# Optimization experiments

Hardware: AMD Instinct MI355X
Metric: run time of the kernel (lower is better)

The kernel has to match this reference:

```python
import jax, jax.numpy as jnp
import numpy as np

EMBED = 768
HIDDEN = 768
HEADS = 12
HEAD_DIM = HIDDEN // HEADS
B, S = 4, 2048


def setup_inputs() -> dict:
    key = jax.random.key(0)
    ks = jax.random.split(key, 12)
    sd = 1.0 / np.sqrt(EMBED)
    return {
        "vector1": jax.random.normal(ks[0], (B, S, EMBED), jnp.float32),
        "vector2": jax.random.normal(ks[1], (B, S, EMBED), jnp.float32),
        "Wq": jax.random.normal(ks[2], (HIDDEN, EMBED), jnp.float32) * sd,
        "bq": jnp.zeros((HIDDEN,), jnp.float32),
        "Wk": jax.random.normal(ks[3], (HIDDEN, EMBED), jnp.float32) * sd,
        "bk": jnp.zeros((HIDDEN,), jnp.float32),
        "Wv": jax.random.normal(ks[4], (HIDDEN, EMBED), jnp.float32) * sd,
        "bv": jnp.zeros((HIDDEN,), jnp.float32),
        "Wo": jax.random.normal(ks[5], (EMBED, HIDDEN), jnp.float32) * sd,
        "bo": jnp.zeros((EMBED,), jnp.float32),
        "alpha": jnp.float32(0.5),
        "beta": jnp.float32(0.5),
    }


def reference(vector1, vector2, Wq, bq, Wk, bk, Wv, bv, Wo, bo, alpha, beta):
    b, s, _ = vector1.shape
    # Linear projections (torch Linear: x @ W.T + b)
    Q = (vector1 @ Wq.T + bq).reshape(b, s, HEADS, HEAD_DIM)  # [B,S,H,D]
    K = (vector2 @ Wk.T + bk).reshape(b, s, HEADS, HEAD_DIM)
    V = (vector2 @ Wv.T + bv).reshape(b, s, HEADS, HEAD_DIM)
    # NOTE: module scales by sqrt(hidden_dim), NOT sqrt(head_dim)
    scale = jnp.float32(np.sqrt(HIDDEN))
    scores = jnp.einsum("bqhd,bkhd->bhqk", Q / scale, K)  # [B,H,S,S]
    # max-subtract + softmax == numerically stable softmax
    attn = jax.nn.softmax(scores, axis=-1)
    out = jnp.einsum("bhqk,bkhd->bqhd", attn, V).reshape(b, s, HIDDEN)
    adjusted = vector1 @ Wo.T + bo
    return alpha * out + beta * adjusted
```

## Files before the change

### kernel.cpp

```cpp
#include <hip/hip_runtime.h>
#include <hip/hip_bf16.h>

#define LOG2E 1.4426950408889634f

typedef __attribute__((ext_vector_type(4)))  float f32x4;
typedef __attribute__((ext_vector_type(16))) float f32x16;
typedef __attribute__((ext_vector_type(8)))  short s16x8;
typedef __attribute__((ext_vector_type(8)))  unsigned short u16x8_t;
typedef __attribute__((ext_vector_type(4)))  int i32x4;

static __device__ __forceinline__ unsigned short f2b(float f) {
    __hip_bfloat16 h = __float2bfloat16(f);
    return __builtin_bit_cast(unsigned short, h);
}

static __device__ __forceinline__ void gload_lds16(const unsigned short* g, unsigned short* l) {
    __builtin_amdgcn_global_load_lds(
        (const __attribute__((address_space(1))) void*)g,
        (__attribute__((address_space(3))) void*)l, 16, 0, 0);
}

__global__ void cvt_f32_to_bf16(const float* __restrict__ src,
                                unsigned short* __restrict__ dst, int n4) {
    int i = blockIdx.x * blockDim.x + threadIdx.x;
    int stride = gridDim.x * blockDim.x;
    for (; i < n4; i += stride) {
        f32x4 v = reinterpret_cast<const f32x4*>(src)[i];
        ushort4 o;
        o.x = f2b(v.x); o.y = f2b(v.y); o.z = f2b(v.z); o.w = f2b(v.w);
        reinterpret_cast<ushort4*>(dst)[i] = o;
    }
}

__global__ void cvt_weights(const float* __restrict__ wq, const float* __restrict__ wk,
                            const float* __restrict__ wv, const float* __restrict__ wo,
                            unsigned short* __restrict__ dst, int quarter4) {
    int i = blockIdx.x * blockDim.x + threadIdx.x;
    int seg = i / quarter4;
    int j = i - seg * quarter4;
    const float* src = (seg == 0) ? wq : (seg == 1) ? wk : (seg == 2) ? wv : wo;
    f32x4 v = reinterpret_cast<const f32x4*>(src)[j];
    ushort4 o;
    o.x = f2b(v.x); o.y = f2b(v.y); o.z = f2b(v.z); o.w = f2b(v.w);
    reinterpret_cast<ushort4*>(dst)[i] = o;
}

__global__ __launch_bounds__(256) void gemm_qkvo(
    const unsigned short* __restrict__ A1,
    const unsigned short* __restrict__ A2,
    const unsigned short* __restrict__ Wcat,
    const float* __restrict__ bq, const float* __restrict__ bk,
    const float* __restrict__ bv, const float* __restrict__ bo,
    unsigned short* __restrict__ Qb,
    unsigned short* __restrict__ Kb,
    unsigned short* __restrict__ Vtb,
    float* __restrict__ adj,
    float qscale)
{
    __shared__ unsigned short As[128 * 64];
    __shared__ unsigned short Bs[128 * 64];

    const int n0g = blockIdx.x * 128;
    const int seg = blockIdx.x / 6;
    const int n0 = n0g - seg * 768;
    const int m0 = blockIdx.y * 128;
    const unsigned short* A = (seg == 1 || seg == 2) ? A2 : A1;
    const float* bias = (seg == 0) ? bq : (seg == 1) ? bk : (seg == 2) ? bv : bo;

    const int tid = threadIdx.x;
    const int w = tid >> 6, lane = tid & 63;
    const int lg = lane >> 4, lr = lane & 15;
    const int wm = w >> 1, wn = w & 1;
    const int srow = tid >> 3;
    const int scol = (tid & 7) * 8;

    const unsigned short* Ag = A    + (size_t)(m0  + srow) * 768 + scol;
    const unsigned short* Bg = Wcat + (size_t)(n0g + srow) * 768 + scol;
    unsigned short* Al = &As[tid * 8];
    unsigned short* Bl = &Bs[tid * 8];

    f32x4 acc[4][4];
#pragma unroll
    for (int i = 0; i < 4; i++)
#pragma unroll
        for (int j = 0; j < 4; j++) acc[i][j] = f32x4{0.f, 0.f, 0.f, 0.f};

    for (int k0 = 0; k0 < 768; k0 += 64) {
#pragma unroll
        for (int c = 0; c < 4; c++) {
            gload_lds16(Ag + c * 32 * 768 + k0, Al + c * 2048);
            gload_lds16(Bg + c * 32 * 768 + k0, Bl + c * 2048);
        }
        __syncthreads();
#pragma unroll
        for (int kk = 0; kk < 2; ++kk) {
            s16x8 af[4], bf[4];
#pragma unroll
            for (int mi = 0; mi < 4; mi++)
                af[mi] = *reinterpret_cast<const s16x8*>(&As[(wm * 64 + mi * 16 + lr) * 64 + kk * 32 + lg * 8]);
#pragma unroll
            for (int ni = 0; ni < 4; ni++)
                bf[ni] = *reinterpret_cast<const s16x8*>(&Bs[(wn * 64 + ni * 16 + lr) * 64 + kk * 32 + lg * 8]);
#pragma unroll
            for (int mi = 0; mi < 4; mi++)
#pragma unroll
                for (int ni = 0; ni < 4; ni++)
                    acc[mi][ni] = __builtin_amdgcn_mfma_f32_16x16x32_bf16(af[mi], bf[ni], acc[mi][ni], 0, 0, 0);
        }
        __syncthreads();
    }

#pragma unroll
    for (int ni = 0; ni < 4; ni++) {
        int n = n0 + wn * 64 + ni * 16 + lr;
        float bn = bias[n];
#pragma unroll
        for (int mi = 0; mi < 4; mi++) {
#pragma unroll
            for (int i = 0; i < 4; i++) {
                int m = m0 + wm * 64 + mi * 16 + 4 * lg + i;
                float v = acc[mi][ni][i] + bn;
                if (seg == 0) {
                    Qb[(size_t)m * 768 + n] = f2b(v * qscale);
                } else if (seg == 1) {
                    Kb[(size_t)m * 768 + n] = f2b(v);
                } else if (seg == 2) {
                    int bb = m >> 11, ss = m & 2047;
                    Vtb[((size_t)(bb * 768 + n) << 11) + ss] = f2b(v);
                } else {
                    adj[(size_t)m * 768 + n] = v;
                }
            }
        }
    }
}

__global__ __launch_bounds__(256, 3) void attn_fused(
    const unsigned short* __restrict__ Qb,
    const unsigned short* __restrict__ Kb,
    const unsigned short* __restrict__ Vt,
    const float* __restrict__ adj,
    const float* __restrict__ alpha_p,
    const float* __restrict__ beta_p,
    float* __restrict__ out)
{
    __shared__ unsigned short Ksm[2][64][72];
    __shared__ unsigned short Vsm[2][64][72];

    const int bh = blockIdx.x;
    const int b = bh / 12, h = bh - 12 * (bh / 12);
    const int tid = threadIdx.x, w = tid >> 6, lane = tid & 63;
    const int ql = lane & 31, hi = lane >> 5;
    const int q0 = blockIdx.y * 128 + w * 32;

    const size_t qbase = ((size_t)(b * 2048 + q0 + ql)) * 768 + h * 64;
    s16x8 qreg[4];
#pragma unroll
    for (int ds = 0; ds < 4; ds++)
        qreg[ds] = *reinterpret_cast<const s16x8*>(Qb + qbase + ds * 16 + hi * 8);

    f32x16 z16;
#pragma unroll
    for (int r = 0; r < 16; r++) z16[r] = 0.f;
    f32x16 acc[2];
#pragma unroll
    for (int dd = 0; dd < 2; dd++) acc[dd] = z16;
    float l = 0.f;

    const size_t kbase = (size_t)b * 2048 * 768 + (size_t)h * 64;
    const size_t vbase = (size_t)(b * 768 + h * 64) * 2048;

    const int krow = tid >> 3, kc8 = (tid & 7) * 8;
    const int vrow = tid >> 3, vc8 = (tid & 7) * 8;

    u16x8_t kst[2], vst[2];
    auto load_tile = [&](int t0) {
#pragma unroll
        for (int i = 0; i < 2; i++)
            kst[i] = *reinterpret_cast<const u16x8_t*>(Kb + kbase + (size_t)(t0 + i * 32 + krow) * 768 + kc8);
#pragma unroll
        for (int i = 0; i < 2; i++)
            vst[i] = *reinterpret_cast<const u16x8_t*>(Vt + vbase + (size_t)(i * 32 + vrow) * 2048 + t0 + vc8);
    };
    auto write_tile = [&](int buf) {
#pragma unroll
        for (int i = 0; i < 2; i++)
            *reinterpret_cast<u16x8_t*>(&Ksm[buf][i * 32 + krow][kc8]) = kst[i];
#pragma unroll
        for (int i = 0; i < 2; i++)
            *reinterpret_cast<u16x8_t*>(&Vsm[buf][i * 32 + vrow][vc8]) = vst[i];
    };

    load_tile(0);
    write_tile(0);
    load_tile(64);
    __syncthreads();

#pragma unroll 1
    for (int t = 0; t < 32; t++) {
        const int cur = t & 1;
        if (t + 1 < 32) write_tile(cur ^ 1);
        if (t + 2 < 32) load_tile((t + 2) * 64);

#pragma unroll
        for (int kb2 = 0; kb2 < 2; kb2++) {
            s16x8 ka0 = *reinterpret_cast<const s16x8*>(&Ksm[cur][kb2 * 32 + ql][0 * 16 + hi * 8]);
            s16x8 ka1 = *reinterpret_cast<const s16x8*>(&Ksm[cur][kb2 * 32 + ql][1 * 16 + hi * 8]);
            s16x8 ka2 = *reinterpret_cast<const s16x8*>(&Ksm[cur][kb2 * 32 + ql][2 * 16 + hi * 8]);
            s16x8 ka3 = *reinterpret_cast<const s16x8*>(&Ksm[cur][kb2 * 32 + ql][3 * 16 + hi * 8]);
            __builtin_amdgcn_s_setprio(1);
            f32x16 sc = __builtin_amdgcn_mfma_f32_32x32x16_bf16(ka0, qreg[0], z16, 0, 0, 0);
            sc = __builtin_amdgcn_mfma_f32_32x32x16_bf16(ka1, qreg[1], sc, 0, 0, 0);
            sc = __builtin_amdgcn_mfma_f32_32x32x16_bf16(ka2, qreg[2], sc, 0, 0, 0);
            sc = __builtin_amdgcn_mfma_f32_32x32x16_bf16(ka3, qreg[3], sc, 0, 0, 0);
            __builtin_amdgcn_s_setprio(0);

            float p[16];
#pragma unroll
            for (int r = 0; r < 16; r++) p[r] = __builtin_exp2f(sc[r]);
            {
                float s0 = p[0] + p[1],  s1 = p[2] + p[3],  s2 = p[4] + p[5],  s3 = p[6] + p[7];
                float s4 = p[8] + p[9],  s5 = p[10] + p[11], s6 = p[12] + p[13], s7 = p[14] + p[15];
                float t0a = s0 + s1, t1a = s2 + s3, t2a = s4 + s5, t3a = s6 + s7;
                l += (t0a + t1a) + (t2a + t3a);
            }

            s16x8 pf[2];
            {
                unsigned int a0, b0, a1, b1, a2, b2, a3, b3;
                asm("v_cvt_pk_bf16_f32 %0, %1, %2" : "=v"(a0) : "v"(p[0]),  "v"(p[1]));
                asm("v_cvt_pk_bf16_f32 %0, %1, %2" : "=v"(b0) : "v"(p[4]),  "v"(p[5]));
                asm("v_cvt_pk_bf16_f32 %0, %1, %2" : "=v"(a1) : "v"(p[2]),  "v"(p[3]));
                asm("v_cvt_pk_bf16_f32 %0, %1, %2" : "=v"(b1) : "v"(p[6]),  "v"(p[7]));
                asm("v_cvt_pk_bf16_f32 %0, %1, %2" : "=v"(a2) : "v"(p[8]),  "v"(p[9]));
                asm("v_cvt_pk_bf16_f32 %0, %1, %2" : "=v"(b2) : "v"(p[12]), "v"(p[13]));
                asm("v_cvt_pk_bf16_f32 %0, %1, %2" : "=v"(a3) : "v"(p[10]), "v"(p[11]));
                asm("v_cvt_pk_bf16_f32 %0, %1, %2" : "=v"(b3) : "v"(p[14]), "v"(p[15]));
                asm volatile("v_permlane32_swap_b32 %0, %1" : "+v"(a0), "+v"(b0));
                asm volatile("v_permlane32_swap_b32 %0, %1" : "+v"(a1), "+v"(b1));
                asm volatile("v_permlane32_swap_b32 %0, %1" : "+v"(a2), "+v"(b2));
                asm volatile("v_permlane32_swap_b32 %0, %1" : "+v"(a3), "+v"(b3));
                i32x4 w0; w0[0] = (int)a0; w0[1] = (int)a1; w0[2] = (int)b0; w0[3] = (int)b1;
                i32x4 w1; w1[0] = (int)a2; w1[1] = (int)a3; w1[2] = (int)b2; w1[3] = (int)b3;
                pf[0] = __builtin_bit_cast(s16x8, w0);
                pf[1] = __builtin_bit_cast(s16x8, w1);
            }

            s16x8 va00 = *reinterpret_cast<const s16x8*>(&Vsm[cur][0 * 32 + ql][kb2 * 32 + 0 * 16 + hi * 8]);
            s16x8 va01 = *reinterpret_cast<const s16x8*>(&Vsm[cur][1 * 32 + ql][kb2 * 32 + 0 * 16 + hi * 8]);
            s16x8 va10 = *reinterpret_cast<const s16x8*>(&Vsm[cur][0 * 32 + ql][kb2 * 32 + 1 * 16 + hi * 8]);
            s16x8 va11 = *reinterpret_cast<const s16x8*>(&Vsm[cur][1 * 32 + ql][kb2 * 32 + 1 * 16 + hi * 8]);
            __builtin_amdgcn_s_setprio(1);
            acc[0] = __builtin_amdgcn_mfma_f32_32x32x16_bf16(va00, pf[0], acc[0], 0, 0, 0);
            acc[1] = __builtin_amdgcn_mfma_f32_32x32x16_bf16(va01, pf[0], acc[1], 0, 0, 0);
            acc[0] = __builtin_amdgcn_mfma_f32_32x32x16_bf16(va10, pf[1], acc[0], 0, 0, 0);
            acc[1] = __builtin_amdgcn_mfma_f32_32x32x16_bf16(va11, pf[1], acc[1], 0, 0, 0);
            __builtin_amdgcn_s_setprio(0);
        }
        __syncthreads();
    }

    l += __shfl_xor(l, 32, 64);

    const float alpha = *alpha_p, beta = *beta_p;
    const float s = alpha / l;
#pragma unroll
    for (int dd = 0; dd < 2; dd++) {
#pragma unroll
        for (int rg = 0; rg < 4; rg++) {
            int d0 = dd * 32 + rg * 8 + hi * 4;
            size_t idx = qbase + d0;
            f32x4 av = *reinterpret_cast<const f32x4*>(adj + idx);
            f32x4 o;
#pragma unroll
            for (int i = 0; i < 4; i++)
                o[i] = acc[dd][rg * 4 + i] * s + beta * av[i];
            *reinterpret_cast<f32x4*>(out + idx) = o;
        }
    }
}

extern "C" void kernel_launch(void* const* d_in, const int* in_sizes, int n_in,
                              void* d_out, int out_size, void* d_ws, size_t ws_size,
                              hipStream_t stream) {
    const float* v1 = (const float*)d_in[0];
    const float* v2 = (const float*)d_in[1];
    const float* Wq = (const float*)d_in[2];
    const float* bq = (const float*)d_in[3];
    const float* Wk = (const float*)d_in[4];
    const float* bk = (const float*)d_in[5];
    const float* Wv = (const float*)d_in[6];
    const float* bv = (const float*)d_in[7];
    const float* Wo = (const float*)d_in[8];
    const float* bo = (const float*)d_in[9];
    const float* alpha = (const float*)d_in[10];
    const float* beta = (const float*)d_in[11];
    float* out = (float*)d_out;

    const size_t ACT = (size_t)8192 * 768;
    const size_t WSZ = (size_t)768 * 768;
    char* ws = (char*)d_ws;
    size_t off = 0;
    auto alloc = [&](size_t bytes) {
        char* p = ws + off;
        off += (bytes + 255) & ~(size_t)255;
        return p;
    };
    unsigned short* v1b  = (unsigned short*)alloc(ACT * 2);
    unsigned short* v2b  = (unsigned short*)alloc(ACT * 2);
    unsigned short* wcat = (unsigned short*)alloc(4 * WSZ * 2);
    unsigned short* Qb   = (unsigned short*)alloc(ACT * 2);
    unsigned short* Kb   = (unsigned short*)alloc(ACT * 2);
    unsigned short* Vtb  = (unsigned short*)alloc(ACT * 2);
    float* adj = (float*)alloc(ACT * 4);

    cvt_f32_to_bf16<<<dim3(1024), dim3(256), 0, stream>>>(v1, v1b, (int)(ACT / 4));
    cvt_f32_to_bf16<<<dim3(1024), dim3(256), 0, stream>>>(v2, v2b, (int)(ACT / 4));
    cvt_weights<<<dim3((int)(4 * WSZ / 4 / 256)), dim3(256), 0, stream>>>(
        Wq, Wk, Wv, Wo, wcat, (int)(WSZ / 4));

    const float qscale = 0.03608439182435161f * 1.4426950408889634f;
    gemm_qkvo<<<dim3(24, 64), dim3(256), 0, stream>>>(
        v1b, v2b, wcat, bq, bk, bv, bo, Qb, Kb, Vtb, adj, qscale);

    attn_fused<<<dim3(48, 16), dim3(256), 0, stream>>>(Qb, Kb, Vtb, adj, alpha, beta, out);
}
```

Baseline: 289.6 us.

## Double-buffer GEMM LDS, remap GEMM blocks across XCDs, give attention waves two query tiles

The QKVO GEMM now uses two LDS buffers, so the next K-slice is staged while the current one is multiplied. It also launches as a 1D grid whose block IDs are remapped so consecutive blocks land on the same XCD. The attention kernel drops to 128 threads, and each wave handles two 32-query fragments. This lets each K/V fragment read from LDS feed twice as many MFMAs, cutting LDS traffic per unit of work. In exchange, register pressure rises and there are fewer waves per CU to hide latency.

```diff
diff --git a/kernel.cpp b/kernel.cpp
--- a/kernel.cpp
+++ b/kernel.cpp
@@ -57,13 +57,17 @@
     float* __restrict__ adj,
     float qscale)
 {
-    __shared__ unsigned short As[128 * 64];
-    __shared__ unsigned short Bs[128 * 64];
-
-    const int n0g = blockIdx.x * 128;
-    const int seg = blockIdx.x / 6;
+    __shared__ unsigned short As[2][128 * 64];
+    __shared__ unsigned short Bs[2][128 * 64];
+
+    const int bid = blockIdx.x;
+    const int wg = (bid & 7) * 192 + (bid >> 3);
+    const int mblk = wg / 24;
+    const int nblk = wg - mblk * 24;
+    const int n0g = nblk * 128;
+    const int seg = nblk / 6;
     const int n0 = n0g - seg * 768;
-    const int m0 = blockIdx.y * 128;
+    const int m0 = mblk * 128;
     const unsigned short* A = (seg == 1 || seg == 2) ? A2 : A1;
     const float* bias = (seg == 0) ? bq : (seg == 1) ? bk : (seg == 2) ? bv : bo;
 
@@ -76,8 +80,14 @@
 
     const unsigned short* Ag = A    + (size_t)(m0  + srow) * 768 + scol;
     const unsigned short* Bg = Wcat + (size_t)(n0g + srow) * 768 + scol;
-    unsigned short* Al = &As[tid * 8];
-    unsigned short* Bl = &Bs[tid * 8];
+
+    auto STAGE = [&](int buf, int k0) {
+#pragma unroll
+        for (int c = 0; c < 4; c++) {
+            gload_lds16(Ag + c * 32 * 768 + k0, &As[buf][tid * 8 + c * 2048]);
+            gload_lds16(Bg + c * 32 * 768 + k0, &Bs[buf][tid * 8 + c * 2048]);
+        }
+    };
 
     f32x4 acc[4][4];
 #pragma unroll
@@ -85,22 +95,22 @@
 #pragma unroll
         for (int j = 0; j < 4; j++) acc[i][j] = f32x4{0.f, 0.f, 0.f, 0.f};
 
-    for (int k0 = 0; k0 < 768; k0 += 64) {
-#pragma unroll
-        for (int c = 0; c < 4; c++) {
-            gload_lds16(Ag + c * 32 * 768 + k0, Al + c * 2048);
-            gload_lds16(Bg + c * 32 * 768 + k0, Bl + c * 2048);
-        }
-        __syncthreads();
+    STAGE(0, 0);
+    __syncthreads();
+
+#pragma unroll 1
+    for (int t = 0; t < 12; t++) {
+        const int curb = t & 1;
+        if (t + 1 < 12) STAGE(curb ^ 1, (t + 1) * 64);
 #pragma unroll
         for (int kk = 0; kk < 2; ++kk) {
             s16x8 af[4], bf[4];
 #pragma unroll
             for (int mi = 0; mi < 4; mi++)
-                af[mi] = *reinterpret_cast<const s16x8*>(&As[(wm * 64 + mi * 16 + lr) * 64 + kk * 32 + lg * 8]);
+                af[mi] = *reinterpret_cast<const s16x8*>(&As[curb][(wm * 64 + mi * 16 + lr) * 64 + kk * 32 + lg * 8]);
 #pragma unroll
             for (int ni = 0; ni < 4; ni++)
-                bf[ni] = *reinterpret_cast<const s16x8*>(&Bs[(wn * 64 + ni * 16 + lr) * 64 + kk * 32 + lg * 8]);
+                bf[ni] = *reinterpret_cast<const s16x8*>(&Bs[curb][(wn * 64 + ni * 16 + lr) * 64 + kk * 32 + lg * 8]);
 #pragma unroll
             for (int mi = 0; mi < 4; mi++)
 #pragma unroll
@@ -135,7 +145,7 @@
     }
 }
 
-__global__ __launch_bounds__(256, 3) void attn_fused(
+__global__ __launch_bounds__(128, 2) void attn_fused(
     const unsigned short* __restrict__ Qb,
     const unsigned short* __restrict__ Kb,
     const unsigned short* __restrict__ Vt,
@@ -151,44 +161,47 @@
     const int b = bh / 12, h = bh - 12 * (bh / 12);
     const int tid = threadIdx.x, w = tid >> 6, lane = tid & 63;
     const int ql = lane & 31, hi = lane >> 5;
-    const int q0 = blockIdx.y * 128 + w * 32;
+    const int q0 = blockIdx.y * 128 + w * 64;
 
     const size_t qbase = ((size_t)(b * 2048 + q0 + ql)) * 768 + h * 64;
-    s16x8 qreg[4];
-#pragma unroll
-    for (int ds = 0; ds < 4; ds++)
-        qreg[ds] = *reinterpret_cast<const s16x8*>(Qb + qbase + ds * 16 + hi * 8);
+    s16x8 qreg[2][4];
+#pragma unroll
+    for (int qf = 0; qf < 2; qf++)
+#pragma unroll
+        for (int ds = 0; ds < 4; ds++)
+            qreg[qf][ds] = *reinterpret_cast<const s16x8*>(Qb + qbase + (size_t)qf * 32 * 768 + ds * 16 + hi * 8);
 
     f32x16 z16;
 #pragma unroll
     for (int r = 0; r < 16; r++) z16[r] = 0.f;
-    f32x16 acc[2];
-#pragma unroll
-    for (int dd = 0; dd < 2; dd++) acc[dd] = z16;
-    float l = 0.f;
+    f32x16 acc[2][2];
+#pragma unroll
+    for (int qf = 0; qf < 2; qf++)
+#pragma unroll
+        for (int dd = 0; dd < 2; dd++) acc[qf][dd] = z16;
+    float l0 = 0.f, l1 = 0.f;
 
     const size_t kbase = (size_t)b * 2048 * 768 + (size_t)h * 64;
     const size_t vbase = (size_t)(b * 768 + h * 64) * 2048;
 
     const int krow = tid >> 3, kc8 = (tid & 7) * 8;
-    const int vrow = tid >> 3, vc8 = (tid & 7) * 8;
-
-    u16x8_t kst[2], vst[2];
+
+    u16x8_t kst[4], vst[4];
     auto load_tile = [&](int t0) {
 #pragma unroll
-        for (int i = 0; i < 2; i++)
-            kst[i] = *reinterpret_cast<const u16x8_t*>(Kb + kbase + (size_t)(t0 + i * 32 + krow) * 768 + kc8);
-#pragma unroll
-        for (int i = 0; i < 2; i++)
-            vst[i] = *reinterpret_cast<const u16x8_t*>(Vt + vbase + (size_t)(i * 32 + vrow) * 2048 + t0 + vc8);
+        for (int i = 0; i < 4; i++)
+            kst[i] = *reinterpret_cast<const u16x8_t*>(Kb + kbase + (size_t)(t0 + i * 16 + krow) * 768 + kc8);
+#pragma unroll
+        for (int i = 0; i < 4; i++)
+            vst[i] = *reinterpret_cast<const u16x8_t*>(Vt + vbase + (size_t)(i * 16 + krow) * 2048 + t0 + kc8);
     };
     auto write_tile = [&](int buf) {
 #pragma unroll
-        for (int i = 0; i < 2; i++)
-            *reinterpret_cast<u16x8_t*>(&Ksm[buf][i * 32 + krow][kc8]) = kst[i];
-#pragma unroll
-        for (int i = 0; i < 2; i++)
-            *reinterpret_cast<u16x8_t*>(&Vsm[buf][i * 32 + vrow][vc8]) = vst[i];
+        for (int i = 0; i < 4; i++)
+            *reinterpret_cast<u16x8_t*>(&Ksm[buf][i * 16 + krow][kc8]) = kst[i];
+#pragma unroll
+        for (int i = 0; i < 4; i++)
+            *reinterpret_cast<u16x8_t*>(&Vsm[buf][i * 16 + krow][kc8]) = vst[i];
     };
 
     load_tile(0);
@@ -208,74 +221,84 @@
             s16x8 ka1 = *reinterpret_cast<const s16x8*>(&Ksm[cur][kb2 * 32 + ql][1 * 16 + hi * 8]);
             s16x8 ka2 = *reinterpret_cast<const s16x8*>(&Ksm[cur][kb2 * 32 + ql][2 * 16 + hi * 8]);
             s16x8 ka3 = *reinterpret_cast<const s16x8*>(&Ksm[cur][kb2 * 32 + ql][3 * 16 + hi * 8]);
-            __builtin_amdgcn_s_setprio(1);
-            f32x16 sc = __builtin_amdgcn_mfma_f32_32x32x16_bf16(ka0, qreg[0], z16, 0, 0, 0);
-            sc = __builtin_amdgcn_mfma_f32_32x32x16_bf16(ka1, qreg[1], sc, 0, 0, 0);
-            sc = __builtin_amdgcn_mfma_f32_32x32x16_bf16(ka2, qreg[2], sc, 0, 0, 0);
-            sc = __builtin_amdgcn_mfma_f32_32x32x16_bf16(ka3, qreg[3], sc, 0, 0, 0);
-            __builtin_amdgcn_s_setprio(0);
-
-            float p[16];
-#pragma unroll
-            for (int r = 0; r < 16; r++) p[r] = __builtin_exp2f(sc[r]);
-            {
-                float s0 = p[0] + p[1],  s1 = p[2] + p[3],  s2 = p[4] + p[5],  s3 = p[6] + p[7];
-                float s4 = p[8] + p[9],  s5 = p[10] + p[11], s6 = p[12] + p[13], s7 = p[14] + p[15];
-                float t0a = s0 + s1, t1a = s2 + s3, t2a = s4 + s5, t3a = s6 + s7;
-                l += (t0a + t1a) + (t2a + t3a);
-            }
-
-            s16x8 pf[2];
-            {
-                unsigned int a0, b0, a1, b1, a2, b2, a3, b3;
-                asm("v_cvt_pk_bf16_f32 %0, %1, %2" : "=v"(a0) : "v"(p[0]),  "v"(p[1]));
-                asm("v_cvt_pk_bf16_f32 %0, %1, %2" : "=v"(b0) : "v"(p[4]),  "v"(p[5]));
-                asm("v_cvt_pk_bf16_f32 %0, %1, %2" : "=v"(a1) : "v"(p[2]),  "v"(p[3]));
-                asm("v_cvt_pk_bf16_f32 %0, %1, %2" : "=v"(b1) : "v"(p[6]),  "v"(p[7]));
-                asm("v_cvt_pk_bf16_f32 %0, %1, %2" : "=v"(a2) : "v"(p[8]),  "v"(p[9]));
-                asm("v_cvt_pk_bf16_f32 %0, %1, %2" : "=v"(b2) : "v"(p[12]), "v"(p[13]));
-                asm("v_cvt_pk_bf16_f32 %0, %1, %2" : "=v"(a3) : "v"(p[10]), "v"(p[11]));
-                asm("v_cvt_pk_bf16_f32 %0, %1, %2" : "=v"(b3) : "v"(p[14]), "v"(p[15]));
-                asm volatile("v_permlane32_swap_b32 %0, %1" : "+v"(a0), "+v"(b0));
-                asm volatile("v_permlane32_swap_b32 %0, %1" : "+v"(a1), "+v"(b1));
-                asm volatile("v_permlane32_swap_b32 %0, %1" : "+v"(a2), "+v"(b2));
-                asm volatile("v_permlane32_swap_b32 %0, %1" : "+v"(a3), "+v"(b3));
-                i32x4 w0; w0[0] = (int)a0; w0[1] = (int)a1; w0[2] = (int)b0; w0[3] = (int)b1;
-                i32x4 w1; w1[0] = (int)a2; w1[1] = (int)a3; w1[2] = (int)b2; w1[3] = (int)b3;
-                pf[0] = __builtin_bit_cast(s16x8, w0);
-                pf[1] = __builtin_bit_cast(s16x8, w1);
-            }
-
             s16x8 va00 = *reinterpret_cast<const s16x8*>(&Vsm[cur][0 * 32 + ql][kb2 * 32 + 0 * 16 + hi * 8]);
             s16x8 va01 = *reinterpret_cast<const s16x8*>(&Vsm[cur][1 * 32 + ql][kb2 * 32 + 0 * 16 + hi * 8]);
             s16x8 va10 = *reinterpret_cast<const s16x8*>(&Vsm[cur][0 * 32 + ql][kb2 * 32 + 1 * 16 + hi * 8]);
             s16x8 va11 = *reinterpret_cast<const s16x8*>(&Vsm[cur][1 * 32 + ql][kb2 * 32 + 1 * 16 + hi * 8]);
-            __builtin_amdgcn_s_setprio(1);
-            acc[0] = __builtin_amdgcn_mfma_f32_32x32x16_bf16(va00, pf[0], acc[0], 0, 0, 0);
-            acc[1] = __builtin_amdgcn_mfma_f32_32x32x16_bf16(va01, pf[0], acc[1], 0, 0, 0);
-            acc[0] = __builtin_amdgcn_mfma_f32_32x32x16_bf16(va10, pf[1], acc[0], 0, 0, 0);
-            acc[1] = __builtin_amdgcn_mfma_f32_32x32x16_bf16(va11, pf[1], acc[1], 0, 0, 0);
-            __builtin_amdgcn_s_setprio(0);
+
+#pragma unroll
+            for (int qf = 0; qf < 2; qf++) {
+                __builtin_amdgcn_s_setprio(1);
+                f32x16 sc = __builtin_amdgcn_mfma_f32_32x32x16_bf16(ka0, qreg[qf][0], z16, 0, 0, 0);
+                sc = __builtin_amdgcn_mfma_f32_32x32x16_bf16(ka1, qreg[qf][1], sc, 0, 0, 0);
+                sc = __builtin_amdgcn_mfma_f32_32x32x16_bf16(ka2, qreg[qf][2], sc, 0, 0, 0);
+                sc = __builtin_amdgcn_mfma_f32_32x32x16_bf16(ka3, qreg[qf][3], sc, 0, 0, 0);
+                __builtin_amdgcn_s_setprio(0);
+
+                float p[16];
+#pragma unroll
+                for (int r = 0; r < 16; r++) p[r] = __builtin_exp2f(sc[r]);
+                {
+                    float s0 = p[0] + p[1],  s1 = p[2] + p[3],  s2 = p[4] + p[5],  s3 = p[6] + p[7];
+                    float s4 = p[8] + p[9],  s5 = p[10] + p[11], s6 = p[12] + p[13], s7 = p[14] + p[15];
+                    float t0a = s0 + s1, t1a = s2 + s3, t2a = s4 + s5, t3a = s6 + s7;
+                    float ls = (t0a + t1a) + (t2a + t3a);
+                    if (qf) l1 += ls; else l0 += ls;
+                }
+
+                s16x8 pf0, pf1;
+                {
+                    unsigned int a0, b0, a1, b1, a2, b2, a3, b3;
+                    asm("v_cvt_pk_bf16_f32 %0, %1, %2" : "=v"(a0) : "v"(p[0]),  "v"(p[1]));
+                    asm("v_cvt_pk_bf16_f32 %0, %1, %2" : "=v"(b0) : "v"(p[4]),  "v"(p[5]));
+                    asm("v_cvt_pk_bf16_f32 %0, %1, %2" : "=v"(a1) : "v"(p[2]),  "v"(p[3]));
+                    asm("v_cvt_pk_bf16_f32 %0, %1, %2" : "=v"(b1) : "v"(p[6]),  "v"(p[7]));
+                    asm("v_cvt_pk_bf16_f32 %0, %1, %2" : "=v"(a2) : "v"(p[8]),  "v"(p[9]));
+                    asm("v_cvt_pk_bf16_f32 %0, %1, %2" : "=v"(b2) : "v"(p[12]), "v"(p[13]));
+                    asm("v_cvt_pk_bf16_f32 %0, %1, %2" : "=v"(a3) : "v"(p[10]), "v"(p[11]));
+                    asm("v_cvt_pk_bf16_f32 %0, %1, %2" : "=v"(b3) : "v"(p[14]), "v"(p[15]));
+                    asm volatile("v_permlane32_swap_b32 %0, %1" : "+v"(a0), "+v"(b0));
+                    asm volatile("v_permlane32_swap_b32 %0, %1" : "+v"(a1), "+v"(b1));
+                    asm volatile("v_permlane32_swap_b32 %0, %1" : "+v"(a2), "+v"(b2));
+                    asm volatile("v_permlane32_swap_b32 %0, %1" : "+v"(a3), "+v"(b3));
+                    i32x4 w0; w0[0] = (int)a0; w0[1] = (int)a1; w0[2] = (int)b0; w0[3] = (int)b1;
+                    i32x4 w1; w1[0] = (int)a2; w1[1] = (int)a3; w1[2] = (int)b2; w1[3] = (int)b3;
+                    pf0 = __builtin_bit_cast(s16x8, w0);
+                    pf1 = __builtin_bit_cast(s16x8, w1);
+                }
+
+                __builtin_amdgcn_s_setprio(1);
+                acc[qf][0] = __builtin_amdgcn_mfma_f32_32x32x16_bf16(va00, pf0, acc[qf][0], 0, 0, 0);
+                acc[qf][1] = __builtin_amdgcn_mfma_f32_32x32x16_bf16(va01, pf0, acc[qf][1], 0, 0, 0);
+                acc[qf][0] = __builtin_amdgcn_mfma_f32_32x32x16_bf16(va10, pf1, acc[qf][0], 0, 0, 0);
+                acc[qf][1] = __builtin_amdgcn_mfma_f32_32x32x16_bf16(va11, pf1, acc[qf][1], 0, 0, 0);
+                __builtin_amdgcn_s_setprio(0);
+            }
         }
         __syncthreads();
     }
 
-    l += __shfl_xor(l, 32, 64);
+    l0 += __shfl_xor(l0, 32, 64);
+    l1 += __shfl_xor(l1, 32, 64);
 
     const float alpha = *alpha_p, beta = *beta_p;
-    const float s = alpha / l;
-#pragma unroll
-    for (int dd = 0; dd < 2; dd++) {
-#pragma unroll
-        for (int rg = 0; rg < 4; rg++) {
-            int d0 = dd * 32 + rg * 8 + hi * 4;
-            size_t idx = qbase + d0;
-            f32x4 av = *reinterpret_cast<const f32x4*>(adj + idx);
-            f32x4 o;
-#pragma unroll
-            for (int i = 0; i < 4; i++)
-                o[i] = acc[dd][rg * 4 + i] * s + beta * av[i];
-            *reinterpret_cast<f32x4*>(out + idx) = o;
+    const float s0v = alpha / l0, s1v = alpha / l1;
+#pragma unroll
+    for (int qf = 0; qf < 2; qf++) {
+        const float sv = qf ? s1v : s0v;
+#pragma unroll
+        for (int dd = 0; dd < 2; dd++) {
+#pragma unroll
+            for (int rg = 0; rg < 4; rg++) {
+                int d0 = dd * 32 + rg * 8 + hi * 4;
+                size_t idx = qbase + (size_t)qf * 32 * 768 + d0;
+                f32x4 av = *reinterpret_cast<const f32x4*>(adj + idx);
+                f32x4 o;
+#pragma unroll
+                for (int i = 0; i < 4; i++)
+                    o[i] = acc[qf][dd][rg * 4 + i] * sv + beta * av[i];
+                *reinterpret_cast<f32x4*>(out + idx) = o;
+            }
         }
     }
 }
@@ -320,8 +343,8 @@
         Wq, Wk, Wv, Wo, wcat, (int)(WSZ / 4));
 
     const float qscale = 0.03608439182435161f * 1.4426950408889634f;
-    gemm_qkvo<<<dim3(24, 64), dim3(256), 0, stream>>>(
+    gemm_qkvo<<<dim3(1536), dim3(256), 0, stream>>>(
         v1b, v2b, wcat, bq, bk, bv, bo, Qb, Kb, Vtb, adj, qscale);
 
-    attn_fused<<<dim3(48, 16), dim3(256), 0, stream>>>(Qb, Kb, Vtb, adj, alpha, beta, out);
-}
+    attn_fused<<<dim3(48, 16), dim3(128), 0, stream>>>(Qb, Kb, Vtb, adj, alpha, beta, out);
+}
```

Result: slower. 309.9 us (+7.0%).

## Split attention over KV halves, double-buffer GEMM LDS, remap GEMM block order

Applied to the files above, without the earlier changes.

Attention is split along the key dimension into two halves (grid z=2), each writing unnormalized partial outputs and row sums. A new combine kernel adds them, normalizes, and applies the alpha/beta blend with the adjusted projection. This doubles the number of attention blocks for better CU occupancy, at the cost of an extra pass over fp32 partials. The projection GEMM now double-buffers its LDS tiles so the next k-slice loads while the current one computes. It also remaps block ids so neighbouring blocks share L2 data, and reuses dead workspace buffers for the partials.

```diff
diff --git a/kernel.cpp b/kernel.cpp
--- a/kernel.cpp
+++ b/kernel.cpp
@@ -1,7 +1,5 @@
 #include <hip/hip_runtime.h>
 #include <hip/hip_bf16.h>
-
-#define LOG2E 1.4426950408889634f
 
 typedef __attribute__((ext_vector_type(4)))  float f32x4;
 typedef __attribute__((ext_vector_type(16))) float f32x16;
@@ -57,13 +55,17 @@
     float* __restrict__ adj,
     float qscale)
 {
-    __shared__ unsigned short As[128 * 64];
-    __shared__ unsigned short Bs[128 * 64];
-
-    const int n0g = blockIdx.x * 128;
-    const int seg = blockIdx.x / 6;
+    __shared__ unsigned short As[2][128 * 64];
+    __shared__ unsigned short Bs[2][128 * 64];
+
+    const int bid = blockIdx.x;
+    const int wg = (bid & 7) * 192 + (bid >> 3);
+    const int mblk = wg / 24;
+    const int nblk = wg - mblk * 24;
+    const int n0g = nblk * 128;
+    const int seg = nblk / 6;
     const int n0 = n0g - seg * 768;
-    const int m0 = blockIdx.y * 128;
+    const int m0 = mblk * 128;
     const unsigned short* A = (seg == 1 || seg == 2) ? A2 : A1;
     const float* bias = (seg == 0) ? bq : (seg == 1) ? bk : (seg == 2) ? bv : bo;
 
@@ -76,8 +78,14 @@
 
     const unsigned short* Ag = A    + (size_t)(m0  + srow) * 768 + scol;
     const unsigned short* Bg = Wcat + (size_t)(n0g + srow) * 768 + scol;
-    unsigned short* Al = &As[tid * 8];
-    unsigned short* Bl = &Bs[tid * 8];
+
+    auto STAGE = [&](int buf, int k0) {
+#pragma unroll
+        for (int c = 0; c < 4; c++) {
+            gload_lds16(Ag + c * 32 * 768 + k0, &As[buf][tid * 8 + c * 2048]);
+            gload_lds16(Bg + c * 32 * 768 + k0, &Bs[buf][tid * 8 + c * 2048]);
+        }
+    };
 
     f32x4 acc[4][4];
 #pragma unroll
@@ -85,22 +93,22 @@
 #pragma unroll
         for (int j = 0; j < 4; j++) acc[i][j] = f32x4{0.f, 0.f, 0.f, 0.f};
 
-    for (int k0 = 0; k0 < 768; k0 += 64) {
-#pragma unroll
-        for (int c = 0; c < 4; c++) {
-            gload_lds16(Ag + c * 32 * 768 + k0, Al + c * 2048);
-            gload_lds16(Bg + c * 32 * 768 + k0, Bl + c * 2048);
-        }
-        __syncthreads();
+    STAGE(0, 0);
+    __syncthreads();
+
+#pragma unroll 1
+    for (int t = 0; t < 12; t++) {
+        const int curb = t & 1;
+        if (t + 1 < 12) STAGE(curb ^ 1, (t + 1) * 64);
 #pragma unroll
         for (int kk = 0; kk < 2; ++kk) {
             s16x8 af[4], bf[4];
 #pragma unroll
             for (int mi = 0; mi < 4; mi++)
-                af[mi] = *reinterpret_cast<const s16x8*>(&As[(wm * 64 + mi * 16 + lr) * 64 + kk * 32 + lg * 8]);
+                af[mi] = *reinterpret_cast<const s16x8*>(&As[curb][(wm * 64 + mi * 16 + lr) * 64 + kk * 32 + lg * 8]);
 #pragma unroll
             for (int ni = 0; ni < 4; ni++)
-                bf[ni] = *reinterpret_cast<const s16x8*>(&Bs[(wn * 64 + ni * 16 + lr) * 64 + kk * 32 + lg * 8]);
+                bf[ni] = *reinterpret_cast<const s16x8*>(&Bs[curb][(wn * 64 + ni * 16 + lr) * 64 + kk * 32 + lg * 8]);
 #pragma unroll
             for (int mi = 0; mi < 4; mi++)
 #pragma unroll
@@ -135,20 +143,25 @@
     }
 }
 
-__global__ __launch_bounds__(256, 3) void attn_fused(
+__global__ __launch_bounds__(256, 4) void attn_partial(
     const unsigned short* __restrict__ Qb,
     const unsigned short* __restrict__ Kb,
     const unsigned short* __restrict__ Vt,
-    const float* __restrict__ adj,
-    const float* __restrict__ alpha_p,
-    const float* __restrict__ beta_p,
-    float* __restrict__ out)
+    float* __restrict__ po0,
+    float* __restrict__ po1,
+    float* __restrict__ lp0,
+    float* __restrict__ lp1)
 {
     __shared__ unsigned short Ksm[2][64][72];
     __shared__ unsigned short Vsm[2][64][72];
 
     const int bh = blockIdx.x;
     const int b = bh / 12, h = bh - 12 * (bh / 12);
+    const int z = blockIdx.z;
+    const int tb = z << 10;
+    float* __restrict__ po = z ? po1 : po0;
+    float* __restrict__ lp = z ? lp1 : lp0;
+
     const int tid = threadIdx.x, w = tid >> 6, lane = tid & 63;
     const int ql = lane & 31, hi = lane >> 5;
     const int q0 = blockIdx.y * 128 + w * 32;
@@ -171,7 +184,6 @@
     const size_t vbase = (size_t)(b * 768 + h * 64) * 2048;
 
     const int krow = tid >> 3, kc8 = (tid & 7) * 8;
-    const int vrow = tid >> 3, vc8 = (tid & 7) * 8;
 
     u16x8_t kst[2], vst[2];
     auto load_tile = [&](int t0) {
@@ -180,7 +192,7 @@
             kst[i] = *reinterpret_cast<const u16x8_t*>(Kb + kbase + (size_t)(t0 + i * 32 + krow) * 768 + kc8);
 #pragma unroll
         for (int i = 0; i < 2; i++)
-            vst[i] = *reinterpret_cast<const u16x8_t*>(Vt + vbase + (size_t)(i * 32 + vrow) * 2048 + t0 + vc8);
+            vst[i] = *reinterpret_cast<const u16x8_t*>(Vt + vbase + (size_t)(i * 32 + krow) * 2048 + t0 + kc8);
     };
     auto write_tile = [&](int buf) {
 #pragma unroll
@@ -188,19 +200,19 @@
             *reinterpret_cast<u16x8_t*>(&Ksm[buf][i * 32 + krow][kc8]) = kst[i];
 #pragma unroll
         for (int i = 0; i < 2; i++)
-            *reinterpret_cast<u16x8_t*>(&Vsm[buf][i * 32 + vrow][vc8]) = vst[i];
+            *reinterpret_cast<u16x8_t*>(&Vsm[buf][i * 32 + krow][kc8]) = vst[i];
     };
 
-    load_tile(0);
+    load_tile(tb);
     write_tile(0);
-    load_tile(64);
+    load_tile(tb + 64);
     __syncthreads();
 
 #pragma unroll 1
-    for (int t = 0; t < 32; t++) {
+    for (int t = 0; t < 16; t++) {
         const int cur = t & 1;
-        if (t + 1 < 32) write_tile(cur ^ 1);
-        if (t + 2 < 32) load_tile((t + 2) * 64);
+        if (t + 1 < 16) write_tile(cur ^ 1);
+        if (t + 2 < 16) load_tile(tb + (t + 2) * 64);
 
 #pragma unroll
         for (int kb2 = 0; kb2 < 2; kb2++) {
@@ -262,22 +274,41 @@
 
     l += __shfl_xor(l, 32, 64);
 
-    const float alpha = *alpha_p, beta = *beta_p;
-    const float s = alpha / l;
 #pragma unroll
     for (int dd = 0; dd < 2; dd++) {
 #pragma unroll
         for (int rg = 0; rg < 4; rg++) {
             int d0 = dd * 32 + rg * 8 + hi * 4;
-            size_t idx = qbase + d0;
-            f32x4 av = *reinterpret_cast<const f32x4*>(adj + idx);
             f32x4 o;
 #pragma unroll
-            for (int i = 0; i < 4; i++)
-                o[i] = acc[dd][rg * 4 + i] * s + beta * av[i];
-            *reinterpret_cast<f32x4*>(out + idx) = o;
-        }
-    }
+            for (int i = 0; i < 4; i++) o[i] = acc[dd][rg * 4 + i];
+            *reinterpret_cast<f32x4*>(po + qbase + d0) = o;
+        }
+    }
+    if (lane < 32) lp[(b * 2048 + q0 + ql) * 12 + h] = l;
+}
+
+__global__ __launch_bounds__(256) void combine_out(
+    const float* __restrict__ po1,
+    const float* __restrict__ lp0, const float* __restrict__ lp1,
+    const float* __restrict__ adj,
+    const float* __restrict__ alpha_p, const float* __restrict__ beta_p,
+    float* __restrict__ out)
+{
+    int i = blockIdx.x * 256 + threadIdx.x;
+    int q = i / 192;
+    int c = i - q * 192;
+    int h = c >> 4;
+    float l = lp0[q * 12 + h] + lp1[q * 12 + h];
+    const float s = (*alpha_p) / l;
+    const float beta = *beta_p;
+    f32x4 a = reinterpret_cast<const f32x4*>(out)[i];
+    f32x4 bq = reinterpret_cast<const f32x4*>(po1)[i];
+    f32x4 ad = reinterpret_cast<const f32x4*>(adj)[i];
+    f32x4 o;
+#pragma unroll
+    for (int j = 0; j < 4; j++) o[j] = (a[j] + bq[j]) * s + beta * ad[j];
+    reinterpret_cast<f32x4*>(out)[i] = o;
 }
 
 extern "C" void kernel_launch(void* const* d_in, const int* in_sizes, int n_in,
@@ -314,14 +345,23 @@
     unsigned short* Vtb  = (unsigned short*)alloc(ACT * 2);
     float* adj = (float*)alloc(ACT * 4);
 
+    float* po1 = (float*)v1b;
+    float* lp0 = (float*)wcat;
+    float* lp1 = lp0 + 8192 * 12;
+    float* po0 = out;
+
     cvt_f32_to_bf16<<<dim3(1024), dim3(256), 0, stream>>>(v1, v1b, (int)(ACT / 4));
     cvt_f32_to_bf16<<<dim3(1024), dim3(256), 0, stream>>>(v2, v2b, (int)(ACT / 4));
     cvt_weights<<<dim3((int)(4 * WSZ / 4 / 256)), dim3(256), 0, stream>>>(
         Wq, Wk, Wv, Wo, wcat, (int)(WSZ / 4));
 
     const float qscale = 0.03608439182435161f * 1.4426950408889634f;
-    gemm_qkvo<<<dim3(24, 64), dim3(256), 0, stream>>>(
+    gemm_qkvo<<<dim3(1536), dim3(256), 0, stream>>>(
         v1b, v2b, wcat, bq, bk, bv, bo, Qb, Kb, Vtb, adj, qscale);
 
-    attn_fused<<<dim3(48, 16), dim3(256), 0, stream>>>(Qb, Kb, Vtb, adj, alpha, beta, out);
-}
+    attn_partial<<<dim3(48, 16, 2), dim3(256), 0, stream>>>(
+        Qb, Kb, Vtb, po0, po1, lp0, lp1);
+
+    combine_out<<<dim3(6144), dim3(256), 0, stream>>>(
+        po1, lp0, lp1, adj, alpha, beta, out);
+}
```

New measurement: 322.4 us. +11.3%, slower.

## Pipeline QKVO GEMM loads in a 4-stage ring, swizzle blocks, compute softmax sum via MFMA

Applied to the files above, without the earlier changes.

The projection GEMM now stages K-slices of 32 through a four-buffer LDS ring using async global-to-LDS loads. It waits on vmcnt counters so loads overlap with MFMA work, instead of syncing twice per 64-wide step. Block IDs are remapped across XCDs so neighbouring tiles share L2. In attention, the softmax row sum moves from VALU adds to an extra MFMA against a ones vector. This trades more matrix-core work for fewer vector instructions and drops the cross-lane shuffle, but the row sum is now accumulated from bf16-rounded probabilities.

```diff
diff --git a/kernel.cpp b/kernel.cpp
--- a/kernel.cpp
+++ b/kernel.cpp
@@ -1,7 +1,5 @@
 #include <hip/hip_runtime.h>
 #include <hip/hip_bf16.h>
-
-#define LOG2E 1.4426950408889634f
 
 typedef __attribute__((ext_vector_type(4)))  float f32x4;
 typedef __attribute__((ext_vector_type(16))) float f32x16;
@@ -57,13 +55,17 @@
     float* __restrict__ adj,
     float qscale)
 {
-    __shared__ unsigned short As[128 * 64];
-    __shared__ unsigned short Bs[128 * 64];
-
-    const int n0g = blockIdx.x * 128;
-    const int seg = blockIdx.x / 6;
+    __shared__ unsigned short As[4 * 128 * 32];
+    __shared__ unsigned short Bs[4 * 128 * 32];
+
+    const int bid = blockIdx.x;
+    const int wg = (bid & 7) * 192 + (bid >> 3);
+    const int mblk = wg / 24;
+    const int nblk = wg - mblk * 24;
+    const int n0g = nblk * 128;
+    const int seg = nblk / 6;
     const int n0 = n0g - seg * 768;
-    const int m0 = blockIdx.y * 128;
+    const int m0 = mblk * 128;
     const unsigned short* A = (seg == 1 || seg == 2) ? A2 : A1;
     const float* bias = (seg == 0) ? bq : (seg == 1) ? bk : (seg == 2) ? bv : bo;
 
@@ -71,13 +73,19 @@
     const int w = tid >> 6, lane = tid & 63;
     const int lg = lane >> 4, lr = lane & 15;
     const int wm = w >> 1, wn = w & 1;
-    const int srow = tid >> 3;
-    const int scol = (tid & 7) * 8;
+    const int srow = tid >> 2;
+    const int scol = (tid & 3) * 8;
 
     const unsigned short* Ag = A    + (size_t)(m0  + srow) * 768 + scol;
     const unsigned short* Bg = Wcat + (size_t)(n0g + srow) * 768 + scol;
-    unsigned short* Al = &As[tid * 8];
-    unsigned short* Bl = &Bs[tid * 8];
+
+    auto STAGE = [&](int buf, int k0) {
+#pragma unroll
+        for (int c = 0; c < 2; c++) {
+            gload_lds16(Ag + (size_t)c * 64 * 768 + k0, &As[buf * 4096 + tid * 8 + c * 2048]);
+            gload_lds16(Bg + (size_t)c * 64 * 768 + k0, &Bs[buf * 4096 + tid * 8 + c * 2048]);
+        }
+    };
 
     f32x4 acc[4][4];
 #pragma unroll
@@ -85,30 +93,41 @@
 #pragma unroll
         for (int j = 0; j < 4; j++) acc[i][j] = f32x4{0.f, 0.f, 0.f, 0.f};
 
-    for (int k0 = 0; k0 < 768; k0 += 64) {
-#pragma unroll
-        for (int c = 0; c < 4; c++) {
-            gload_lds16(Ag + c * 32 * 768 + k0, Al + c * 2048);
-            gload_lds16(Bg + c * 32 * 768 + k0, Bl + c * 2048);
-        }
-        __syncthreads();
-#pragma unroll
-        for (int kk = 0; kk < 2; ++kk) {
-            s16x8 af[4], bf[4];
-#pragma unroll
-            for (int mi = 0; mi < 4; mi++)
-                af[mi] = *reinterpret_cast<const s16x8*>(&As[(wm * 64 + mi * 16 + lr) * 64 + kk * 32 + lg * 8]);
+    auto COMPUTE = [&](int buf) {
+        s16x8 af[4], bf[4];
+#pragma unroll
+        for (int mi = 0; mi < 4; mi++)
+            af[mi] = *reinterpret_cast<const s16x8*>(&As[buf * 4096 + (wm * 64 + mi * 16 + lr) * 32 + lg * 8]);
+#pragma unroll
+        for (int ni = 0; ni < 4; ni++)
+            bf[ni] = *reinterpret_cast<const s16x8*>(&Bs[buf * 4096 + (wn * 64 + ni * 16 + lr) * 32 + lg * 8]);
+#pragma unroll
+        for (int mi = 0; mi < 4; mi++)
 #pragma unroll
             for (int ni = 0; ni < 4; ni++)
-                bf[ni] = *reinterpret_cast<const s16x8*>(&Bs[(wn * 64 + ni * 16 + lr) * 64 + kk * 32 + lg * 8]);
-#pragma unroll
-            for (int mi = 0; mi < 4; mi++)
-#pragma unroll
-                for (int ni = 0; ni < 4; ni++)
-                    acc[mi][ni] = __builtin_amdgcn_mfma_f32_16x16x32_bf16(af[mi], bf[ni], acc[mi][ni], 0, 0, 0);
-        }
-        __syncthreads();
-    }
+                acc[mi][ni] = __builtin_amdgcn_mfma_f32_16x16x32_bf16(af[mi], bf[ni], acc[mi][ni], 0, 0, 0);
+    };
+
+    STAGE(0, 0);
+    STAGE(1, 32);
+    STAGE(2, 64);
+
+#pragma unroll 1
+    for (int t = 0; t < 22; t++) {
+        asm volatile("s_waitcnt vmcnt(8)" ::: "memory");
+        __builtin_amdgcn_sched_barrier(0);
+        __builtin_amdgcn_s_barrier();
+        if (t + 3 < 24) STAGE((t + 3) & 3, (t + 3) * 32);
+        COMPUTE(t & 3);
+    }
+    asm volatile("s_waitcnt vmcnt(4)" ::: "memory");
+    __builtin_amdgcn_sched_barrier(0);
+    __builtin_amdgcn_s_barrier();
+    COMPUTE(22 & 3);
+    asm volatile("s_waitcnt vmcnt(0)" ::: "memory");
+    __builtin_amdgcn_sched_barrier(0);
+    __builtin_amdgcn_s_barrier();
+    COMPUTE(23 & 3);
 
 #pragma unroll
     for (int ni = 0; ni < 4; ni++) {
@@ -159,19 +178,22 @@
     for (int ds = 0; ds < 4; ds++)
         qreg[ds] = *reinterpret_cast<const s16x8*>(Qb + qbase + ds * 16 + hi * 8);
 
+    s16x8 ones;
+#pragma unroll
+    for (int j = 0; j < 8; j++) ones[j] = (short)0x3F80;
+
     f32x16 z16;
 #pragma unroll
     for (int r = 0; r < 16; r++) z16[r] = 0.f;
     f32x16 acc[2];
 #pragma unroll
     for (int dd = 0; dd < 2; dd++) acc[dd] = z16;
-    float l = 0.f;
+    f32x16 acc_l = z16;
 
     const size_t kbase = (size_t)b * 2048 * 768 + (size_t)h * 64;
     const size_t vbase = (size_t)(b * 768 + h * 64) * 2048;
 
     const int krow = tid >> 3, kc8 = (tid & 7) * 8;
-    const int vrow = tid >> 3, vc8 = (tid & 7) * 8;
 
     u16x8_t kst[2], vst[2];
     auto load_tile = [&](int t0) {
@@ -180,7 +202,7 @@
             kst[i] = *reinterpret_cast<const u16x8_t*>(Kb + kbase + (size_t)(t0 + i * 32 + krow) * 768 + kc8);
 #pragma unroll
         for (int i = 0; i < 2; i++)
-            vst[i] = *reinterpret_cast<const u16x8_t*>(Vt + vbase + (size_t)(i * 32 + vrow) * 2048 + t0 + vc8);
+            vst[i] = *reinterpret_cast<const u16x8_t*>(Vt + vbase + (size_t)(i * 32 + krow) * 2048 + t0 + kc8);
     };
     auto write_tile = [&](int buf) {
 #pragma unroll
@@ -188,7 +210,7 @@
             *reinterpret_cast<u16x8_t*>(&Ksm[buf][i * 32 + krow][kc8]) = kst[i];
 #pragma unroll
         for (int i = 0; i < 2; i++)
-            *reinterpret_cast<u16x8_t*>(&Vsm[buf][i * 32 + vrow][vc8]) = vst[i];
+            *reinterpret_cast<u16x8_t*>(&Vsm[buf][i * 32 + krow][kc8]) = vst[i];
     };
 
     load_tile(0);
@@ -218,12 +240,6 @@
             float p[16];
 #pragma unroll
             for (int r = 0; r < 16; r++) p[r] = __builtin_exp2f(sc[r]);
-            {
-                float s0 = p[0] + p[1],  s1 = p[2] + p[3],  s2 = p[4] + p[5],  s3 = p[6] + p[7];
-                float s4 = p[8] + p[9],  s5 = p[10] + p[11], s6 = p[12] + p[13], s7 = p[14] + p[15];
-                float t0a = s0 + s1, t1a = s2 + s3, t2a = s4 + s5, t3a = s6 + s7;
-                l += (t0a + t1a) + (t2a + t3a);
-            }
 
             s16x8 pf[2];
             {
@@ -253,15 +269,16 @@
             __builtin_amdgcn_s_setprio(1);
             acc[0] = __builtin_amdgcn_mfma_f32_32x32x16_bf16(va00, pf[0], acc[0], 0, 0, 0);
             acc[1] = __builtin_amdgcn_mfma_f32_32x32x16_bf16(va01, pf[0], acc[1], 0, 0, 0);
+            acc_l  = __builtin_amdgcn_mfma_f32_32x32x16_bf16(ones, pf[0], acc_l, 0, 0, 0);
             acc[0] = __builtin_amdgcn_mfma_f32_32x32x16_bf16(va10, pf[1], acc[0], 0, 0, 0);
             acc[1] = __builtin_amdgcn_mfma_f32_32x32x16_bf16(va11, pf[1], acc[1], 0, 0, 0);
+            acc_l  = __builtin_amdgcn_mfma_f32_32x32x16_bf16(ones, pf[1], acc_l, 0, 0, 0);
             __builtin_amdgcn_s_setprio(0);
         }
         __syncthreads();
     }
 
-    l += __shfl_xor(l, 32, 64);
-
+    const float l = acc_l[0];
     const float alpha = *alpha_p, beta = *beta_p;
     const float s = alpha / l;
 #pragma unroll
@@ -320,7 +337,7 @@
         Wq, Wk, Wv, Wo, wcat, (int)(WSZ / 4));
 
     const float qscale = 0.03608439182435161f * 1.4426950408889634f;
-    gemm_qkvo<<<dim3(24, 64), dim3(256), 0, stream>>>(
+    gemm_qkvo<<<dim3(1536), dim3(256), 0, stream>>>(
         v1b, v2b, wcat, bq, bk, bv, bo, Qb, Kb, Vtb, adj, qscale);
 
     attn_fused<<<dim3(48, 16), dim3(256), 0, stream>>>(Qb, Kb, Vtb, adj, alpha, beta, out);
```

Result: faster. 280.5 us (-3.1%).
